# Optimization experiments

Hardware: AMD Instinct MI355X
Metric: run time of the kernel (lower is better)

Reference implementation:

```python
import jax, jax.numpy as jnp
import numpy as np
from jax import lax

B, HP, WP, C, HEADS, SR = 8, 128, 128, 128, 2, 8
HEAD_DIM = C // HEADS
SCALE = HEAD_DIM ** -0.5
LN_EPS = 1e-5


def setup_inputs() -> dict:
    key = jax.random.key(0)
    ks = jax.random.split(key, 6)
    s = 0.02
    N = HP * WP
    return {
        "x": jax.random.normal(ks[0], (B, N, C), jnp.float32),
        "Hp": HP,
        "Wp": WP,
        "q_w": jax.random.normal(ks[1], (C, C), jnp.float32) * s,
        "q_b": jnp.zeros((C,), jnp.float32),
        "kv_w": jax.random.normal(ks[2], (2 * C, C), jnp.float32) * s,
        "kv_b": jnp.zeros((2 * C,), jnp.float32),
        "sr_w": jax.random.normal(ks[3], (C, C, SR, SR), jnp.float32) * s,  # OIHW
        "ln_g": jnp.ones((C,), jnp.float32),
        "ln_b": jnp.zeros((C,), jnp.float32),
        "proj_w": jax.random.normal(ks[4], (C, C), jnp.float32) * s,
        "proj_b": jnp.zeros((C,), jnp.float32),
    }


def reference(x, Hp, Wp, q_w, q_b, kv_w, kv_b, sr_w, ln_g, ln_b, proj_w, proj_b):
    Bn, N, Cd = x.shape
    # Q from full tokens: [B, H, N, hd]
    q = (x @ q_w.T + q_b).reshape(Bn, N, HEADS, HEAD_DIM).transpose(0, 2, 1, 3)
    # spatial reduction: conv kernel=stride=SR, no bias
    t2d = x.transpose(0, 2, 1).reshape(Bn, Cd, Hp, Wp)  # NCHW
    t2d = lax.conv_general_dilated(
        t2d, sr_w, window_strides=(SR, SR), padding="VALID",
        dimension_numbers=("NCHW", "OIHW", "NCHW"))
    Nk = t2d.shape[2] * t2d.shape[3]
    tok_kv = t2d.reshape(Bn, Cd, Nk).transpose(0, 2, 1)  # [B, Nk, C]
    # LayerNorm over channel dim
    mu = jnp.mean(tok_kv, axis=-1, keepdims=True)
    var = jnp.mean(jnp.square(tok_kv - mu), axis=-1, keepdims=True)
    tok_kv = (tok_kv - mu) * lax.rsqrt(var + LN_EPS) * ln_g + ln_b
    # K, V: [B, H, Nk, hd]
    kv = (tok_kv @ kv_w.T + kv_b).reshape(Bn, Nk, 2, HEADS, HEAD_DIM)
    kv = kv.transpose(2, 0, 3, 1, 4)
    k, v = kv[0], kv[1]
    # attention
    attn = jnp.einsum("bhnd,bhmd->bhnm", q, k) * SCALE
    attn = jax.nn.softmax(attn, axis=-1)
    out = jnp.einsum("bhnm,bhmd->bhnd", attn, v)
    out = out.transpose(0, 2, 1, 3).reshape(Bn, N, Cd)
    return out @ proj_w.T + proj_b
```

## Files before the change

kernel.cpp:

```cpp
#include <hip/hip_runtime.h>
#include <cstdint>

#define BB 8
#define NN 16384
#define CC 128
#define HEADS 2
#define HD 64
#define NK 256

#define OFF_CF   0
#define OFF_KVF  524288
#define OFF_QF   540672
#define OFF_PF   548864
#define OFF_K    557056
#define OFF_V    819200
#define OFF_PART 1081344

typedef __attribute__((ext_vector_type(8))) __bf16 bf16x8;
typedef __attribute__((ext_vector_type(16))) float f32x16;
typedef __attribute__((ext_vector_type(4))) float f32x4;

union U4 { uint32_t u[4]; uint4 q; bf16x8 v; };

__device__ __forceinline__ uint32_t cvt_pk_bf16(float lo, float hi) {
  uint32_t r;
  asm("v_cvt_pk_bf16_f32 %0, %1, %2" : "=v"(r) : "v"(lo), "v"(hi));
  return r;
}
__device__ __forceinline__ void permswap(uint32_t& a, uint32_t& b) {
  asm("v_permlane32_swap_b32 %0, %1" : "+v"(a), "+v"(b));
}

__global__ __launch_bounds__(256) void prep_w(
    const float* __restrict__ sr_w, const float* __restrict__ proj_w,
    const float* __restrict__ kv_w, const float* __restrict__ q_w,
    float* __restrict__ ws) {
  int tid = blockIdx.x * 256 + threadIdx.x;
  if (tid < 524288) {
    int u = tid;
    int jp = u & 3, l = (u >> 2) & 63, nt = (u >> 8) & 7, ks = u >> 11;
    int k = ks * 32 + ((l >> 4) & 3) * 8 + jp * 2;
    int o = nt * 16 + (l & 15);
    int c = k & 127, p = k >> 7;
    ((uint32_t*)(ws + OFF_CF))[u] =
        cvt_pk_bf16(sr_w[o * 8192 + c * 64 + p], sr_w[o * 8192 + (c + 1) * 64 + p]);
  } else if (tid < 540672) {
    int u = tid - 524288;
    int jp = u & 3, l = (u >> 2) & 63, nt = (u >> 8) & 15, ks = u >> 12;
    int k = ks * 32 + ((l >> 4) & 3) * 8 + jp * 2;
    int o = nt * 16 + (l & 15);
    ((uint32_t*)(ws + OFF_KVF))[u] = cvt_pk_bf16(kv_w[o * 128 + k], kv_w[o * 128 + k + 1]);
  } else if (tid < 548864) {
    int u = tid - 540672;
    int jp = u & 3, l = (u >> 2) & 63, nt = (u >> 8) & 3, ks = u >> 10;
    int k = ks * 16 + (l >> 5) * 8 + jp * 2;
    int o = nt * 32 + (l & 31);
    ((uint32_t*)(ws + OFF_QF))[u] = cvt_pk_bf16(q_w[o * 128 + k], q_w[o * 128 + k + 1]);
  } else {
    int u = tid - 548864;
    int jp = u & 3, l = (u >> 2) & 63, nt = (u >> 8) & 3, ks = u >> 10;
    int k = ks * 16 + (l >> 5) * 8 + jp * 2;
    int o = nt * 32 + (l & 31);
    ((uint32_t*)(ws + OFF_PF))[u] = cvt_pk_bf16(proj_w[o * 128 + k], proj_w[o * 128 + k + 1]);
  }
}

template<int NSUB>
__global__ __launch_bounds__(512, 2) void conv_partial(
    const float* __restrict__ x, const uint32_t* __restrict__ cf,
    float* __restrict__ partial) {
  extern __shared__ __align__(16) char lds[];
  const int t = threadIdx.x;
  const int l = t & 63, w = t >> 6;
  const int NQ = 8 / NSUB;
  const int tile = blockIdx.x / NQ;
  const int khq  = blockIdx.x % NQ;
  const int b  = tile >> 4;
  const int ti = tile & 15;
  char* sreg = lds + w * 4096;
  const int col = l & 15, kg = (l >> 4) & 3;

  f32x4 acc[8];
  #pragma unroll
  for (int nt = 0; nt < 8; ++nt) acc[nt] = (f32x4)0.0f;

  #pragma unroll
  for (int si = 0; si < NSUB; ++si) {
    const int sub = khq * NSUB + si;
    #pragma unroll
    for (int it = 0; it < 4; ++it) {
      int flat = it * 64 + l;
      int tk = flat >> 4, c16 = flat & 15;
      const float* src = x + ((size_t)b * NN + ((ti * 8 + w) * 128 + tk * 8 + sub)) * CC + c16 * 8;
      float4 a0 = *(const float4*)(src);
      float4 a1 = *(const float4*)(src + 4);
      U4 pk;
      pk.u[0] = cvt_pk_bf16(a0.x, a0.y); pk.u[1] = cvt_pk_bf16(a0.z, a0.w);
      pk.u[2] = cvt_pk_bf16(a1.x, a1.y); pk.u[3] = cvt_pk_bf16(a1.z, a1.w);
      *(uint4*)(sreg + tk * 256 + ((c16 * 16) ^ ((tk & 7) << 4))) = pk.q;
    }
    const int ksg0 = (w * 8 + sub) * 4;
    #pragma unroll
    for (int ksl = 0; ksl < 4; ++ksl) {
      U4 a;
      a.q = *(const uint4*)(sreg + col * 256 + ((ksl * 64 + kg * 16) ^ ((col & 7) << 4)));
      #pragma unroll
      for (int nt = 0; nt < 8; ++nt) {
        U4 bf_;
        bf_.q = *(const uint4*)(cf + (((ksg0 + ksl) * 8 + nt) * 64 + l) * 4);
        acc[nt] = __builtin_amdgcn_mfma_f32_16x16x32_bf16(a.v, bf_.v, acc[nt], 0, 0, 0);
      }
    }
  }

  float* rbuf = (float*)(lds + 32768);
  if (w >= 4) {
    float* dst = rbuf + (w - 4) * 2048;
    #pragma unroll
    for (int nt = 0; nt < 8; ++nt)
      #pragma unroll
      for (int r = 0; r < 4; ++r) dst[(kg * 4 + r) * 128 + nt * 16 + col] = acc[nt][r];
  }
  __syncthreads();
  if (w < 4) {
    const float* s1 = rbuf + w * 2048;
    #pragma unroll
    for (int nt = 0; nt < 8; ++nt)
      #pragma unroll
      for (int r = 0; r < 4; ++r) acc[nt][r] += s1[(kg * 4 + r) * 128 + nt * 16 + col];
    if (w >= 2) {
      float* dst = rbuf + w * 2048;
      #pragma unroll
      for (int nt = 0; nt < 8; ++nt)
        #pragma unroll
        for (int r = 0; r < 4; ++r) dst[(kg * 4 + r) * 128 + nt * 16 + col] = acc[nt][r];
    }
  }
  __syncthreads();
  if (w < 2) {
    const float* s2 = rbuf + (w + 2) * 2048;
    #pragma unroll
    for (int nt = 0; nt < 8; ++nt)
      #pragma unroll
      for (int r = 0; r < 4; ++r) acc[nt][r] += s2[(kg * 4 + r) * 128 + nt * 16 + col];
    if (w == 1) {
      float* dst = rbuf + 2048;
      #pragma unroll
      for (int nt = 0; nt < 8; ++nt)
        #pragma unroll
        for (int r = 0; r < 4; ++r) dst[(kg * 4 + r) * 128 + nt * 16 + col] = acc[nt][r];
    }
  }
  __syncthreads();
  if (w == 0) {
    const float* s3 = rbuf + 2048;
    #pragma unroll
    for (int nt = 0; nt < 8; ++nt)
      #pragma unroll
      for (int r = 0; r < 4; ++r) {
        acc[nt][r] += s3[(kg * 4 + r) * 128 + nt * 16 + col];
        rbuf[(kg * 4 + r) * 128 + nt * 16 + col] = acc[nt][r];
      }
  }
  __syncthreads();
  float4 vv = ((const float4*)rbuf)[t];
  ((float4*)(partial + ((size_t)khq * 128 + tile) * 2048))[t] = vv;
}

__global__ __launch_bounds__(512) void reduce_ln_kv(
    const float* __restrict__ partial, int nq,
    const uint32_t* __restrict__ kvf, const float* __restrict__ kv_b,
    const float* __restrict__ ln_g, const float* __restrict__ ln_b,
    float* __restrict__ kbuf, float* __restrict__ vbuf) {
  __shared__ __align__(16) char abuf[4096];
  const int t = threadIdx.x;
  const int l = t & 63, w = t >> 6;
  const int tile = blockIdx.x;
  const int b = tile >> 4, nk0 = (tile & 15) * 16;

  float4 a = make_float4(0.f, 0.f, 0.f, 0.f);
  for (int i = 0; i < nq; ++i) {
    float4 p = *(const float4*)(partial + ((size_t)i * 128 + tile) * 2048 + t * 4);
    a.x += p.x; a.y += p.y; a.z += p.z; a.w += p.w;
  }
  {
    const int tk = t >> 5, j = t & 31;
    float s  = a.x + a.y + a.z + a.w;
    float ss = a.x * a.x + a.y * a.y + a.z * a.z + a.w * a.w;
    #pragma unroll
    for (int m = 16; m; m >>= 1) { s += __shfl_xor(s, m); ss += __shfl_xor(ss, m); }
    float mu  = s * 0.0078125f;
    float var = fmaxf(ss * 0.0078125f - mu * mu, 0.f);
    float rs  = rsqrtf(var + 1e-5f);
    float4 g4 = *(const float4*)(ln_g + j * 4);
    float4 b4 = *(const float4*)(ln_b + j * 4);
    float y0 = (a.x - mu) * rs * g4.x + b4.x;
    float y1 = (a.y - mu) * rs * g4.y + b4.y;
    float y2 = (a.z - mu) * rs * g4.z + b4.z;
    float y3 = (a.w - mu) * rs * g4.w + b4.w;
    *(uint2*)(abuf + tk * 256 + ((j * 8) ^ ((tk & 7) << 4))) =
        make_uint2(cvt_pk_bf16(y0, y1), cvt_pk_bf16(y2, y3));
  }
  __syncthreads();

  const int col = l & 15, kg = (l >> 4) & 3;
  f32x4 kacc[2];
  kacc[0] = (f32x4)0.0f; kacc[1] = (f32x4)0.0f;
  #pragma unroll
  for (int ks = 0; ks < 4; ++ks) {
    U4 aa;
    aa.q = *(const uint4*)(abuf + col * 256 + ((ks * 64 + kg * 16) ^ ((col & 7) << 4)));
    #pragma unroll
    for (int i = 0; i < 2; ++i) {
      int nt = w * 2 + i;
      U4 bf_;
      bf_.q = *(const uint4*)(kvf + ((ks * 16 + nt) * 64 + l) * 4);
      kacc[i] = __builtin_amdgcn_mfma_f32_16x16x32_bf16(aa.v, bf_.v, kacc[i], 0, 0, 0);
    }
  }
  #pragma unroll
  for (int i = 0; i < 2; ++i) {
    int kvo = (w * 2 + i) * 16 + col;
    float bias = kv_b[kvo];
    float* obuf = (kvo >= 128) ? vbuf : kbuf;
    int h = (kvo >> 6) & 1, d = kvo & 63;
    #pragma unroll
    for (int r = 0; r < 4; ++r) {
      int tkr = kg * 4 + r;
      obuf[(((size_t)b * HEADS + h) * NK + nk0 + tkr) * HD + d] = kacc[i][r] + bias;
    }
  }
}

__global__ __launch_bounds__(256) void gemm128(
    const float* X, const uint32_t* __restrict__ frags,
    const float* __restrict__ bias, float scale, float* Y) {
  const int t = threadIdx.x;
  const int l = t & 63, wid = t >> 6;
  const int lq = l & 31, lh = l >> 5;
  const size_t rowbase = (size_t)blockIdx.x * 128 + wid * 32;
  const float* xrow = X + (rowbase + lq) * CC;
  f32x16 acc[4];
  #pragma unroll
  for (int nt = 0; nt < 4; ++nt) acc[nt] = (f32x16)0.0f;
  #pragma unroll
  for (int ks = 0; ks < 8; ++ks) {
    float4 a0 = *(const float4*)(xrow + ks * 16 + lh * 8);
    float4 a1 = *(const float4*)(xrow + ks * 16 + lh * 8 + 4);
    U4 af;
    af.u[0] = cvt_pk_bf16(a0.x, a0.y); af.u[1] = cvt_pk_bf16(a0.z, a0.w);
    af.u[2] = cvt_pk_bf16(a1.x, a1.y); af.u[3] = cvt_pk_bf16(a1.z, a1.w);
    #pragma unroll
    for (int nt = 0; nt < 4; ++nt) {
      U4 bf_;
      bf_.q = *(const uint4*)(frags + ((ks * 4 + nt) * 64 + l) * 4);
      acc[nt] = __builtin_amdgcn_mfma_f32_32x32x16_bf16(af.v, bf_.v, acc[nt], 0, 0, 0);
    }
  }
  #pragma unroll
  for (int nt = 0; nt < 4; ++nt) {
    int o = nt * 32 + lq;
    float bv = bias[o];
    #pragma unroll
    for (int r = 0; r < 16; ++r) {
      int m = (r & 3) + 8 * (r >> 2) + 4 * lh;
      Y[(rowbase + m) * CC + o] = (acc[nt][r] + bv) * scale;
    }
  }
}

__global__ __launch_bounds__(256, 2) void attn_mfma(
    const float* __restrict__ qsrc, const float* __restrict__ kbuf,
    const float* __restrict__ vbuf, float* __restrict__ out) {
  __shared__ __align__(16) char lds[65536];
  const int t  = threadIdx.x;
  const int l  = t & 63, wid = t >> 6;
  const int lq = l & 31, lh = l >> 5;
  const int bh = blockIdx.x >> 7;
  const int b  = bh >> 1, h = bh & 1;
  const int qbase = (blockIdx.x & 127) * 128;

  U4 qb[4];
  {
    const float* q0 = qsrc + ((size_t)b * NN + qbase + wid * 32 + lq) * CC + h * 64;
    #pragma unroll
    for (int kg = 0; kg < 4; ++kg) {
      float4 x0 = *(const float4*)(q0 + kg * 16 + lh * 8);
      float4 x1 = *(const float4*)(q0 + kg * 16 + lh * 8 + 4);
      qb[kg].u[0] = cvt_pk_bf16(x0.x, x0.y); qb[kg].u[1] = cvt_pk_bf16(x0.z, x0.w);
      qb[kg].u[2] = cvt_pk_bf16(x1.x, x1.y); qb[kg].u[3] = cvt_pk_bf16(x1.z, x1.w);
    }
  }

  {
    const float* kb = kbuf + (size_t)bh * NK * HD;
    #pragma unroll
    for (int it = 0; it < 16; ++it) {
      int flat = it * 256 + t;
      int key = flat >> 4, j = flat & 15;
      float4 kv = *(const float4*)(kb + key * HD + j * 4);
      int byte = (key * 128 + j * 8) ^ ((key & 7) << 4);
      *(uint2*)(lds + byte) = make_uint2(cvt_pk_bf16(kv.x, kv.y), cvt_pk_bf16(kv.z, kv.w));
    }
    const float* vb = vbuf + (size_t)bh * NK * HD;
    int d = t & 63, kb4 = t >> 6;
    #pragma unroll
    for (int k0 = 0; k0 < 64; k0 += 4) {
      int k = kb4 * 64 + k0;
      float v0 = vb[(k + 0) * HD + d], v1 = vb[(k + 1) * HD + d];
      float v2 = vb[(k + 2) * HD + d], v3 = vb[(k + 3) * HD + d];
      int byte = 32768 + ((d * 512 + k * 2) ^ ((d & 7) << 4));
      *(uint2*)(lds + byte) = make_uint2(cvt_pk_bf16(v0, v1), cvt_pk_bf16(v2, v3));
    }
  }
  __syncthreads();

  f32x16 p[8];
  #pragma unroll
  for (int kt = 0; kt < 8; ++kt) p[kt] = (f32x16)0.0f;
  #pragma unroll
  for (int kt = 0; kt < 8; ++kt) {
    const int key = kt * 32 + lq;
    #pragma unroll
    for (int kg = 0; kg < 4; ++kg) {
      U4 a;
      int byte = (key * 128 + kg * 32 + lh * 16) ^ ((key & 7) << 4);
      a.q = *(const uint4*)(lds + byte);
      p[kt] = __builtin_amdgcn_mfma_f32_32x32x16_bf16(a.v, qb[kg].v, p[kt], 0, 0, 0);
    }
  }

  float mx = -1e30f;
  #pragma unroll
  for (int kt = 0; kt < 8; ++kt)
    #pragma unroll
    for (int i = 0; i < 16; ++i) mx = fmaxf(mx, p[kt][i]);
  mx = fmaxf(mx, __shfl_xor(mx, 32));
  float sum = 0.f;
  #pragma unroll
  for (int kt = 0; kt < 8; ++kt)
    #pragma unroll
    for (int i = 0; i < 16; ++i) { float e = __expf(p[kt][i] - mx); p[kt][i] = e; sum += e; }
  sum += __shfl_xor(sum, 32);
  const float inv = 1.f / sum;
  #pragma unroll
  for (int kt = 0; kt < 8; ++kt)
    #pragma unroll
    for (int i = 0; i < 16; ++i) p[kt][i] *= inv;

  f32x16 oacc0 = (f32x16)0.0f, oacc1 = (f32x16)0.0f;
  #pragma unroll
  for (int kt = 0; kt < 8; ++kt) {
    uint32_t x0 = cvt_pk_bf16(p[kt][0],  p[kt][1]);
    uint32_t x1 = cvt_pk_bf16(p[kt][2],  p[kt][3]);
    uint32_t y0 = cvt_pk_bf16(p[kt][4],  p[kt][5]);
    uint32_t y1 = cvt_pk_bf16(p[kt][6],  p[kt][7]);
    permswap(x0, y0); permswap(x1, y1);
    U4 pa0; pa0.u[0] = x0; pa0.u[1] = x1; pa0.u[2] = y0; pa0.u[3] = y1;
    uint32_t x2 = cvt_pk_bf16(p[kt][8],  p[kt][9]);
    uint32_t x3 = cvt_pk_bf16(p[kt][10], p[kt][11]);
    uint32_t y2 = cvt_pk_bf16(p[kt][12], p[kt][13]);
    uint32_t y3 = cvt_pk_bf16(p[kt][14], p[kt][15]);
    permswap(x2, y2); permswap(x3, y3);
    U4 pa1; pa1.u[0] = x2; pa1.u[1] = x3; pa1.u[2] = y2; pa1.u[3] = y3;
    #pragma unroll
    for (int dt = 0; dt < 2; ++dt) {
      int d = dt * 32 + lq;
      U4 vb0, vb1;
      int byte0 = 32768 + ((d * 512 + kt * 64 + lh * 16) ^ ((d & 7) << 4));
      int byte1 = 32768 + ((d * 512 + kt * 64 + 32 + lh * 16) ^ ((d & 7) << 4));
      vb0.q = *(const uint4*)(lds + byte0);
      vb1.q = *(const uint4*)(lds + byte1);
      f32x16& oa = dt ? oacc1 : oacc0;
      oa = __builtin_amdgcn_mfma_f32_32x32x16_bf16(pa0.v, vb0.v, oa, 0, 0, 0);
      oa = __builtin_amdgcn_mfma_f32_32x32x16_bf16(pa1.v, vb1.v, oa, 0, 0, 0);
    }
  }

  float* ob = out + ((size_t)b * NN + qbase + wid * 32) * CC + h * 64;
  #pragma unroll
  for (int reg = 0; reg < 16; ++reg) {
    int q = (reg & 3) + 8 * (reg >> 2) + 4 * lh;
    ob[q * CC + lq]      = oacc0[reg];
    ob[q * CC + 32 + lq] = oacc1[reg];
  }
}

extern "C" void kernel_launch(void* const* d_in, const int* in_sizes, int n_in,
                              void* d_out, int out_size, void* d_ws, size_t ws_size,
                              hipStream_t stream) {
  const float* x      = (const float*)d_in[0];
  const float* q_w    = (const float*)d_in[3];
  const float* q_b    = (const float*)d_in[4];
  const float* kv_w   = (const float*)d_in[5];
  const float* kv_b   = (const float*)d_in[6];
  const float* sr_w   = (const float*)d_in[7];
  const float* ln_g   = (const float*)d_in[8];
  const float* ln_b   = (const float*)d_in[9];
  const float* proj_w = (const float*)d_in[10];
  const float* proj_b = (const float*)d_in[11];
  float* out = (float*)d_out;
  float* ws  = (float*)d_ws;

  prep_w<<<dim3(2176), dim3(256), 0, stream>>>(sr_w, proj_w, kv_w, q_w, ws);

  int nq = 1;
  if (ws_size >= (size_t)(OFF_PART + 8 * 262144) * 4) nq = 8;
  else if (ws_size >= (size_t)(OFF_PART + 4 * 262144) * 4) nq = 4;
  else if (ws_size >= (size_t)(OFF_PART + 2 * 262144) * 4) nq = 2;

  const uint32_t* cf = (const uint32_t*)(ws + OFF_CF);
  float* part = ws + OFF_PART;
  if (nq == 8)
    conv_partial<1><<<dim3(1024), dim3(512), 65536, stream>>>(x, cf, part);
  else if (nq == 4)
    conv_partial<2><<<dim3(512), dim3(512), 65536, stream>>>(x, cf, part);
  else if (nq == 2)
    conv_partial<4><<<dim3(256), dim3(512), 65536, stream>>>(x, cf, part);
  else
    conv_partial<8><<<dim3(128), dim3(512), 65536, stream>>>(x, cf, part);

  reduce_ln_kv<<<dim3(128), dim3(512), 0, stream>>>(
      part, nq, (const uint32_t*)(ws + OFF_KVF), kv_b, ln_g, ln_b,
      ws + OFF_K, ws + OFF_V);
  gemm128<<<dim3(1024), dim3(256), 0, stream>>>(
      x, (const uint32_t*)(ws + OFF_QF), q_b, 0.125f, out);
  attn_mfma<<<dim3(2048), dim3(256), 0, stream>>>(
      out, ws + OFF_K, ws + OFF_V, out);
  gemm128<<<dim3(1024), dim3(256), 0, stream>>>(
      out, (const uint32_t*)(ws + OFF_PF), proj_b, 1.0f, out);
}
```

Measured before the change: 130.0 us.

## Recompute QK scores in a second pass to cut attention register pressure

The attention kernel no longer keeps all 8 score tiles in registers. A first pass computes QK^T only to find the row max. A second pass recomputes the scores, exponentiates them and feeds them straight into the PV MFMAs, and the softmax normalisation is applied at the end through a small shared-memory table of inverse sums. Launch bounds go from 2 to 3 blocks per CU to use the lower register demand. The cost is twice the QK MFMA and LDS read work, plus an extra barrier. Occupancy may still be capped by the roughly 64 KB of LDS each block uses.

```diff
diff --git a/kernel.cpp b/kernel.cpp
--- a/kernel.cpp
+++ b/kernel.cpp
@@ -269,10 +269,11 @@
   }
 }
 
-__global__ __launch_bounds__(256, 2) void attn_mfma(
+__global__ __launch_bounds__(256, 3) void attn_mfma2p(
     const float* __restrict__ qsrc, const float* __restrict__ kbuf,
     const float* __restrict__ vbuf, float* __restrict__ out) {
   __shared__ __align__(16) char lds[65536];
+  __shared__ float sinv[4][32];
   const int t  = threadIdx.x;
   const int l  = t & 63, wid = t >> 6;
   const int lq = l & 31, lh = l >> 5;
@@ -315,52 +316,49 @@
   }
   __syncthreads();
 
-  f32x16 p[8];
-  #pragma unroll
-  for (int kt = 0; kt < 8; ++kt) p[kt] = (f32x16)0.0f;
+  float mx = -1e30f;
   #pragma unroll
   for (int kt = 0; kt < 8; ++kt) {
+    f32x16 s = (f32x16)0.0f;
     const int key = kt * 32 + lq;
     #pragma unroll
     for (int kg = 0; kg < 4; ++kg) {
       U4 a;
       int byte = (key * 128 + kg * 32 + lh * 16) ^ ((key & 7) << 4);
       a.q = *(const uint4*)(lds + byte);
-      p[kt] = __builtin_amdgcn_mfma_f32_32x32x16_bf16(a.v, qb[kg].v, p[kt], 0, 0, 0);
-    }
-  }
-
-  float mx = -1e30f;
-  #pragma unroll
-  for (int kt = 0; kt < 8; ++kt)
-    #pragma unroll
-    for (int i = 0; i < 16; ++i) mx = fmaxf(mx, p[kt][i]);
+      s = __builtin_amdgcn_mfma_f32_32x32x16_bf16(a.v, qb[kg].v, s, 0, 0, 0);
+    }
+    #pragma unroll
+    for (int i = 0; i < 16; ++i) mx = fmaxf(mx, s[i]);
+  }
   mx = fmaxf(mx, __shfl_xor(mx, 32));
+
   float sum = 0.f;
-  #pragma unroll
-  for (int kt = 0; kt < 8; ++kt)
-    #pragma unroll
-    for (int i = 0; i < 16; ++i) { float e = __expf(p[kt][i] - mx); p[kt][i] = e; sum += e; }
-  sum += __shfl_xor(sum, 32);
-  const float inv = 1.f / sum;
-  #pragma unroll
-  for (int kt = 0; kt < 8; ++kt)
-    #pragma unroll
-    for (int i = 0; i < 16; ++i) p[kt][i] *= inv;
-
   f32x16 oacc0 = (f32x16)0.0f, oacc1 = (f32x16)0.0f;
   #pragma unroll
   for (int kt = 0; kt < 8; ++kt) {
-    uint32_t x0 = cvt_pk_bf16(p[kt][0],  p[kt][1]);
-    uint32_t x1 = cvt_pk_bf16(p[kt][2],  p[kt][3]);
-    uint32_t y0 = cvt_pk_bf16(p[kt][4],  p[kt][5]);
-    uint32_t y1 = cvt_pk_bf16(p[kt][6],  p[kt][7]);
+    f32x16 s = (f32x16)0.0f;
+    const int key = kt * 32 + lq;
+    #pragma unroll
+    for (int kg = 0; kg < 4; ++kg) {
+      U4 a;
+      int byte = (key * 128 + kg * 32 + lh * 16) ^ ((key & 7) << 4);
+      a.q = *(const uint4*)(lds + byte);
+      s = __builtin_amdgcn_mfma_f32_32x32x16_bf16(a.v, qb[kg].v, s, 0, 0, 0);
+    }
+    #pragma unroll
+    for (int i = 0; i < 16; ++i) { float e = __expf(s[i] - mx); s[i] = e; sum += e; }
+
+    uint32_t x0 = cvt_pk_bf16(s[0],  s[1]);
+    uint32_t x1 = cvt_pk_bf16(s[2],  s[3]);
+    uint32_t y0 = cvt_pk_bf16(s[4],  s[5]);
+    uint32_t y1 = cvt_pk_bf16(s[6],  s[7]);
     permswap(x0, y0); permswap(x1, y1);
     U4 pa0; pa0.u[0] = x0; pa0.u[1] = x1; pa0.u[2] = y0; pa0.u[3] = y1;
-    uint32_t x2 = cvt_pk_bf16(p[kt][8],  p[kt][9]);
-    uint32_t x3 = cvt_pk_bf16(p[kt][10], p[kt][11]);
-    uint32_t y2 = cvt_pk_bf16(p[kt][12], p[kt][13]);
-    uint32_t y3 = cvt_pk_bf16(p[kt][14], p[kt][15]);
+    uint32_t x2 = cvt_pk_bf16(s[8],  s[9]);
+    uint32_t x3 = cvt_pk_bf16(s[10], s[11]);
+    uint32_t y2 = cvt_pk_bf16(s[12], s[13]);
+    uint32_t y3 = cvt_pk_bf16(s[14], s[15]);
     permswap(x2, y2); permswap(x3, y3);
     U4 pa1; pa1.u[0] = x2; pa1.u[1] = x3; pa1.u[2] = y2; pa1.u[3] = y3;
     #pragma unroll
@@ -375,6 +373,17 @@
       oa = __builtin_amdgcn_mfma_f32_32x32x16_bf16(pa0.v, vb0.v, oa, 0, 0, 0);
       oa = __builtin_amdgcn_mfma_f32_32x32x16_bf16(pa1.v, vb1.v, oa, 0, 0, 0);
     }
+  }
+  sum += __shfl_xor(sum, 32);
+  if (l < 32) sinv[wid][lq] = 1.f / sum;
+  __syncthreads();
+
+  #pragma unroll
+  for (int reg = 0; reg < 16; ++reg) {
+    int q = (reg & 3) + 8 * (reg >> 2) + 4 * lh;
+    float iv = sinv[wid][q];
+    oacc0[reg] *= iv;
+    oacc1[reg] *= iv;
   }
 
   float* ob = out + ((size_t)b * NN + qbase + wid * 32) * CC + h * 64;
@@ -425,7 +434,7 @@
       ws + OFF_K, ws + OFF_V);
   gemm128<<<dim3(1024), dim3(256), 0, stream>>>(
       x, (const uint32_t*)(ws + OFF_QF), q_b, 0.125f, out);
-  attn_mfma<<<dim3(2048), dim3(256), 0, stream>>>(
+  attn_mfma2p<<<dim3(2048), dim3(256), 0, stream>>>(
       out, ws + OFF_K, ws + OFF_V, out);
   gemm128<<<dim3(1024), dim3(256), 0, stream>>>(
       out, (const uint32_t*)(ws + OFF_PF), proj_b, 1.0f, out);
```

Result: no change. 130.3 us (+0.2%).
